# Kernel optimization log

Hardware: AMD Instinct MI355X
Metric: run time of the kernel (lower is better)

Reference implementation:

```python
import jax, jax.numpy as jnp
import numpy as np

N_NODES = 10000
N_EDGES = 160000
MUL = 64            # multiplicity of 0e and 1o in node features
AVG_NEIGH = 16.0    # avg_num_neighbors
N_BESSEL = 8
NUM_IRREPS = 4 * MUL  # 2*MUL scalars (0e) + 2*MUL vectors (1o) after concat+regroup

# e3nn normalize2mom constant for swish: 1/sqrt(E_{z~N(0,1)}[swish(z)^2])
_z, _w = np.polynomial.hermite_e.hermegauss(128)
_silu = _z / (1.0 + np.exp(-_z))
ACT_C = float(1.0 / np.sqrt(np.sum(_w * _silu ** 2) / np.sqrt(2.0 * np.pi)))


def bessel(x, n=N_BESSEL):
    # e3nn.bessel with x_max=1: sqrt(2) * sin(k*pi*x)/x, k=1..n
    k = jnp.arange(1, n + 1, dtype=x.dtype)
    xs = jnp.where(x == 0.0, 1.0, x)[:, None]
    return jnp.sqrt(2.0) * jnp.where(x[:, None] == 0.0, k * jnp.pi, jnp.sin(jnp.pi * k * xs) / xs)


def envelope(x):
    return jnp.where(x < 1.0, 1.0 - 28.0 * x ** 6 + 48.0 * x ** 7 - 21.0 * x ** 8, 0.0)


def mlp(x, Ws):
    # e3nn MultiLayerPerceptron: y = x @ W / sqrt(fan_in), normalized swish on hidden layers
    n = len(Ws)
    for i, W in enumerate(Ws):
        x = x @ W / jnp.sqrt(jnp.asarray(W.shape[0], x.dtype))
        if i < n - 1:
            x = ACT_C * jax.nn.swish(x)
    return x


def setup_inputs() -> dict:
    key = jax.random.key(0)
    ks = jax.random.split(key, 8)
    vectors = 0.35 * jax.random.normal(ks[0], (N_EDGES, 3), jnp.float32)
    node_scalars = jax.random.normal(ks[1], (N_NODES, MUL), jnp.float32)
    node_vectors = jax.random.normal(ks[2], (N_NODES, MUL, 3), jnp.float32)
    senders = jax.random.randint(ks[3], (N_EDGES,), 0, N_NODES)
    receivers = jax.random.randint(ks[4], (N_EDGES,), 0, N_NODES)
    W1 = jax.random.normal(ks[5], (N_BESSEL, 64), jnp.float32)
    W2 = jax.random.normal(ks[6], (64, 64), jnp.float32)
    W3 = jax.random.normal(ks[7], (64, NUM_IRREPS), jnp.float32)
    return dict(vectors=vectors, node_scalars=node_scalars, node_vectors=node_vectors,
                senders=senders, receivers=receivers, W1=W1, W2=W2, W3=W3)


def reference(vectors, node_scalars, node_vectors, senders, receivers, W1, W2, W3):
    lengths = jnp.linalg.norm(vectors, axis=-1, keepdims=True)        # [E,1]
    Y1 = jnp.sqrt(3.0) * vectors / lengths                            # component-normalized l=1 SH [E,3]

    # gather sender features
    m0 = node_scalars[senders]                                        # [E,MUL]   0e
    m1 = node_vectors[senders]                                        # [E,MUL,3] 1o

    # CG tensor product with Y1, filtered to target irreps (0e + 1o), component norm
    tp0 = jnp.einsum('eui,ei->eu', m1, Y1) / jnp.sqrt(3.0)            # 1o x 1o -> 0e
    tp1 = m0[:, :, None] * Y1[:, None, :]                             # 0e x 1o -> 1o

    s = jnp.concatenate([m0, tp0], axis=1)                            # [E,2*MUL]
    v = jnp.concatenate([m1, tp1], axis=1)                            # [E,2*MUL,3]

    # radial embedding -> per-irrep gates
    x = lengths[:, 0]
    radial = bessel(x) * envelope(x)[:, None]                         # [E,8]
    mix = mlp(radial, (W1, W2, W3))                                   # [E,4*MUL]

    s = s * mix[:, : 2 * MUL]
    v = v * mix[:, 2 * MUL :, None]

    # scatter-add to receivers
    out_s = jax.ops.segment_sum(s, receivers, num_segments=N_NODES)   # [N,2*MUL]
    out_v = jax.ops.segment_sum(v, receivers, num_segments=N_NODES)   # [N,2*MUL,3]
    inv = 1.0 / jnp.sqrt(AVG_NEIGH)
    return jnp.concatenate([out_s * inv, (out_v * inv).reshape(N_NODES, -1)], axis=1)
```

## Files before the change

kernel.cpp:

```cpp
#include <hip/hip_runtime.h>
#include <hip/hip_fp16.h>
#include <math.h>

#define N_NODES 10000
#define N_EDGES 160000
#define TBL_N 126
#define ACT_C 1.676518f
#define CAP 64
#define S3 1.7320508075688772f

#define SCAT_BLOCKS 625
#define CONV_BLOCKS 2500
#define TBL_BLOCKS  32
#define GATHER_BLOCKS 512
#define GATHER_THREADS 512

__device__ uint2  g_tbl[(TBL_N + 1) * 64];
__device__ uint2  g_nd2[N_NODES * 64];
__device__ int    g_cnt[N_NODES];
__device__ float4 g_bkt[N_NODES * CAP];

__device__ __forceinline__ float2 h2f(unsigned int v) {
    __half2 h = *(__half2*)&v;
    return __half22float2(h);
}

__global__ __launch_bounds__(256) void prep_scatter(
    const float* __restrict__ W1, const float* __restrict__ W2, const float* __restrict__ W3,
    const float* __restrict__ node_scalars, const float* __restrict__ node_vectors,
    const float* __restrict__ vectors, const int* __restrict__ senders,
    const int* __restrict__ receivers)
{
    const int bx = (int)blockIdx.x;
    const int tid = threadIdx.x;
    const int lane = tid & 63;
    const int wl = tid >> 6;

    if (bx < SCAT_BLOCKS) {
        int e = bx * 256 + tid;
        if (e < N_EDGES) {
            float vx = vectors[3 * e], vy = vectors[3 * e + 1], vz = vectors[3 * e + 2];
            float x2 = vx * vx + vy * vy + vz * vz;
            if (x2 < 1.0f) {
                float invx = rsqrtf(x2);
                float x = x2 * invx;
                float t = x * (float)TBL_N;
                int idx = (int)t;            if (idx > TBL_N - 1) idx = TBL_N - 1;
                int fr  = (int)((t - (float)idx) * 512.0f);  if (fr > 511) fr = 511;
                unsigned int bits = ((unsigned int)senders[e] << 16) |
                                    ((unsigned int)idx << 9) | (unsigned int)fr;
                int r = receivers[e];
                int slot = atomicAdd(&g_cnt[r], 1);
                if (slot < CAP)
                    g_bkt[(r << 6) + slot] =
                        make_float4(vx * invx, vy * invx, vz * invx, __uint_as_float(bits));
            }
        }
        return;
    }
    if (bx < SCAT_BLOCKS + CONV_BLOCKS) {
        int n = (bx - SCAT_BLOCKS) * 4 + wl;
        float m0 = node_scalars[n * 64 + lane];
        const float* p = node_vectors + n * 192 + 3 * lane;
        __half2 h01 = __floats2half2_rn(m0, p[0]);
        __half2 h23 = __floats2half2_rn(p[1], p[2]);
        uint2 r;
        r.x = *(unsigned int*)&h01;
        r.y = *(unsigned int*)&h23;
        g_nd2[n * 64 + lane] = r;
        return;
    }

    __shared__ float h[4][64];
    int wid = (bx - SCAT_BLOCKS - CONV_BLOCKS) * 4 + wl;
    if (wid > TBL_N) wid = TBL_N;
    const float x = (float)wid * (1.0f / (float)TBL_N);
    float x2 = x * x, x3 = x2 * x, x6 = x3 * x3;
    float env = (x < 1.0f) ? (1.0f - 28.0f * x6 + 48.0f * x6 * x - 21.0f * x6 * x2) : 0.0f;
    const float pi = 3.14159265358979f;
    float radial[8];
    #pragma unroll
    for (int k = 1; k <= 8; ++k) {
        float b = (x == 0.0f) ? ((float)k * pi) : (sinf(pi * (float)k * x) / x);
        radial[k - 1] = 1.41421356237f * b * env;
    }
    float acc = 0.0f;
    #pragma unroll
    for (int k = 0; k < 8; ++k) acc += radial[k] * W1[k * 64 + lane];
    acc *= 0.35355339059f;
    float a = ACT_C * acc / (1.0f + expf(-acc));
    h[wl][lane] = a;
    __syncthreads();
    acc = 0.0f;
    #pragma unroll 8
    for (int k = 0; k < 64; ++k) acc += h[wl][k] * W2[k * 64 + lane];
    acc *= 0.125f;
    a = ACT_C * acc / (1.0f + expf(-acc));
    __syncthreads();
    h[wl][lane] = a;
    __syncthreads();
    float m0 = 0.f, m1 = 0.f, m2 = 0.f, m3 = 0.f;
    #pragma unroll 4
    for (int k = 0; k < 64; ++k) {
        float hk = h[wl][k];
        const float* w = W3 + k * 256 + lane;
        m0 += hk * w[0];
        m1 += hk * w[64];
        m2 += hk * w[128];
        m3 += hk * w[192];
    }
    __half2 h01 = __floats2half2_rn(m0 * 0.125f, m1 * 0.125f);
    __half2 h23 = __floats2half2_rn(m2 * 0.125f, m3 * 0.125f);
    uint2 r;
    r.x = *(unsigned int*)&h01;
    r.y = *(unsigned int*)&h23;
    g_tbl[wid * 64 + lane] = r;
}

__device__ __forceinline__ void edge_math(uint2 q0, uint2 q1, uint2 nv, float f,
                                          float yx, float yy, float yz,
                                          float& accA, float& accB,
                                          float& aCx, float& aCy, float& aCz,
                                          float& aDx, float& aDy, float& aDz) {
    float2 a0 = h2f(q0.x);
    float2 b0 = h2f(q0.y);
    float2 a1 = h2f(q1.x);
    float2 b1 = h2f(q1.y);
    float2 p01 = h2f(nv.x);
    float2 p23 = h2f(nv.y);

    float mA = fmaf(f, a1.x - a0.x, a0.x);
    float mB = fmaf(f, a1.y - a0.y, a0.y);
    float mC = fmaf(f, b1.x - b0.x, b0.x);
    float mD = fmaf(f, b1.y - b0.y, b0.y);

    float m0u = p01.x, vx = p01.y, vy = p23.x, vzv = p23.y;
    float tp0 = fmaf(vx, yx, fmaf(vy, yy, vzv * yz));
    accA = fmaf(m0u, mA, accA);
    accB = fmaf(tp0, mB, accB);
    aCx = fmaf(mC, vx,  aCx);
    aCy = fmaf(mC, vy,  aCy);
    aCz = fmaf(mC, vzv, aCz);
    float cD = m0u * mD * S3;
    aDx = fmaf(cD, yx, aDx);
    aDy = fmaf(cD, yy, aDy);
    aDz = fmaf(cD, yz, aDz);
}

__global__ __launch_bounds__(GATHER_THREADS) void gather_kernel(float* __restrict__ out) {
    __shared__ uint2 tbl[(TBL_N + 1) * 64];
    const int tid = threadIdx.x;
    for (int i = tid; i < (TBL_N + 1) * 64; i += GATHER_THREADS)
        tbl[i] = g_tbl[i];
    __syncthreads();

    const int u = tid & 63;
    const int w = tid >> 6;
    const int nwaves = GATHER_BLOCKS * 8;

    for (int n = (int)blockIdx.x * 8 + w; n < N_NODES; n += nwaves) {
        int cnt = g_cnt[n]; if (cnt > CAP) cnt = CAP;
        const int base = n << 6;
        const float4 myrec = g_bkt[base + (u < cnt ? u : 0)];

        float accA = 0.f, accB = 0.f;
        float aCx = 0.f, aCy = 0.f, aCz = 0.f;
        float aDx = 0.f, aDy = 0.f, aDz = 0.f;

        int j = 0;
        for (; j + 4 <= cnt; j += 4) {
            uint2 q0[4], q1[4], nv[4];
            float yx[4], yy[4], yz[4], f[4];
            #pragma unroll
            for (int k = 0; k < 4; ++k) {
                int jj = j + k;
                yx[k] = __shfl(myrec.x, jj);
                yy[k] = __shfl(myrec.y, jj);
                yz[k] = __shfl(myrec.z, jj);
                unsigned int bits = __float_as_uint(__shfl(myrec.w, jj));
                int sv = (int)(bits >> 16);
                int i  = (int)((bits >> 9) & 127u);
                f[k] = (float)(bits & 511u) * (1.0f / 512.0f);
                q0[k] = tbl[i * 64 + u];
                q1[k] = tbl[i * 64 + 64 + u];
                nv[k] = g_nd2[sv * 64 + u];
            }
            #pragma unroll
            for (int k = 0; k < 4; ++k)
                edge_math(q0[k], q1[k], nv[k], f[k], yx[k], yy[k], yz[k],
                          accA, accB, aCx, aCy, aCz, aDx, aDy, aDz);
        }
        for (; j < cnt; ++j) {
            float yx = __shfl(myrec.x, j);
            float yy = __shfl(myrec.y, j);
            float yz = __shfl(myrec.z, j);
            unsigned int bits = __float_as_uint(__shfl(myrec.w, j));
            int sv = (int)(bits >> 16);
            int i  = (int)((bits >> 9) & 127u);
            float f = (float)(bits & 511u) * (1.0f / 512.0f);
            edge_math(tbl[i * 64 + u], tbl[i * 64 + 64 + u], g_nd2[sv * 64 + u], f,
                      yx, yy, yz, accA, accB, aCx, aCy, aCz, aDx, aDy, aDz);
        }

        const float inv = 0.25f;
        float* o = out + (size_t)n * 512;
        o[u]       = inv * accA;
        o[64 + u]  = inv * accB;
        o[128 + 3 * u + 0] = inv * aCx;
        o[128 + 3 * u + 1] = inv * aCy;
        o[128 + 3 * u + 2] = inv * aCz;
        o[320 + 3 * u + 0] = inv * aDx;
        o[320 + 3 * u + 1] = inv * aDy;
        o[320 + 3 * u + 2] = inv * aDz;
        if (u == 0) g_cnt[n] = 0;
    }
}

extern "C" void kernel_launch(void* const* d_in, const int* in_sizes, int n_in,
                              void* d_out, int out_size, void* d_ws, size_t ws_size,
                              hipStream_t stream) {
    const float* vectors      = (const float*)d_in[0];
    const float* node_scalars = (const float*)d_in[1];
    const float* node_vectors = (const float*)d_in[2];
    const int*   senders      = (const int*)d_in[3];
    const int*   receivers    = (const int*)d_in[4];
    const float* W1           = (const float*)d_in[5];
    const float* W2           = (const float*)d_in[6];
    const float* W3           = (const float*)d_in[7];
    float* out = (float*)d_out;

    prep_scatter<<<SCAT_BLOCKS + CONV_BLOCKS + TBL_BLOCKS, 256, 0, stream>>>(
        W1, W2, W3, node_scalars, node_vectors, vectors, senders, receivers);
    gather_kernel<<<GATHER_BLOCKS, GATHER_THREADS, 0, stream>>>(out);
}
```

Baseline: 45.29 us.

## Halve radial table resolution, double gather blocks, batch eight sender loads per step

The radial lookup table is cut from 127 to 64 rows, which halves the shared-memory footprint per gather block. Together with a launch-bounds occupancy hint and twice as many gather blocks, this is meant to fit more blocks per CU. The gather loop now issues eight sender-node loads up front, with clamped tail indices, before doing the edge math. The aim is more outstanding memory requests to hide gather latency. The coarser table interpolation reduces accuracy, and the bucket record is now loaded unconditionally even for slots beyond the count.

```diff
diff --git a/kernel.cpp b/kernel.cpp
--- a/kernel.cpp
+++ b/kernel.cpp
@@ -4,18 +4,19 @@
 
 #define N_NODES 10000
 #define N_EDGES 160000
-#define TBL_N 126
+#define TBL_N 63
+#define TBL_ROWS 64
 #define ACT_C 1.676518f
 #define CAP 64
 #define S3 1.7320508075688772f
 
 #define SCAT_BLOCKS 625
 #define CONV_BLOCKS 2500
-#define TBL_BLOCKS  32
-#define GATHER_BLOCKS 512
+#define TBL_BLOCKS  16
+#define GATHER_BLOCKS 1024
 #define GATHER_THREADS 512
 
-__device__ uint2  g_tbl[(TBL_N + 1) * 64];
+__device__ uint2  g_tbl[TBL_ROWS * 64];
 __device__ uint2  g_nd2[N_NODES * 64];
 __device__ int    g_cnt[N_NODES];
 __device__ float4 g_bkt[N_NODES * CAP];
@@ -73,7 +74,6 @@
 
     __shared__ float h[4][64];
     int wid = (bx - SCAT_BLOCKS - CONV_BLOCKS) * 4 + wl;
-    if (wid > TBL_N) wid = TBL_N;
     const float x = (float)wid * (1.0f / (float)TBL_N);
     float x2 = x * x, x3 = x2 * x, x6 = x3 * x3;
     float env = (x < 1.0f) ? (1.0f - 28.0f * x6 + 48.0f * x6 * x - 21.0f * x6 * x2) : 0.0f;
@@ -147,10 +147,10 @@
     aDz = fmaf(cD, yz, aDz);
 }
 
-__global__ __launch_bounds__(GATHER_THREADS) void gather_kernel(float* __restrict__ out) {
-    __shared__ uint2 tbl[(TBL_N + 1) * 64];
+__global__ __launch_bounds__(GATHER_THREADS, 8) void gather_kernel(float* __restrict__ out) {
+    __shared__ uint2 tbl[TBL_ROWS * 64];
     const int tid = threadIdx.x;
-    for (int i = tid; i < (TBL_N + 1) * 64; i += GATHER_THREADS)
+    for (int i = tid; i < TBL_ROWS * 64; i += GATHER_THREADS)
         tbl[i] = g_tbl[i];
     __syncthreads();
 
@@ -159,47 +159,37 @@
     const int nwaves = GATHER_BLOCKS * 8;
 
     for (int n = (int)blockIdx.x * 8 + w; n < N_NODES; n += nwaves) {
-        int cnt = g_cnt[n]; if (cnt > CAP) cnt = CAP;
         const int base = n << 6;
-        const float4 myrec = g_bkt[base + (u < cnt ? u : 0)];
+        int cnt = g_cnt[n];
+        const float4 myrec = g_bkt[base + u];
+        if (cnt > CAP) cnt = CAP;
 
         float accA = 0.f, accB = 0.f;
         float aCx = 0.f, aCy = 0.f, aCz = 0.f;
         float aDx = 0.f, aDy = 0.f, aDz = 0.f;
 
-        int j = 0;
-        for (; j + 4 <= cnt; j += 4) {
-            uint2 q0[4], q1[4], nv[4];
-            float yx[4], yy[4], yz[4], f[4];
+        for (int j = 0; j < cnt; j += 8) {
+            uint2 nv[8];
             #pragma unroll
-            for (int k = 0; k < 4; ++k) {
-                int jj = j + k;
-                yx[k] = __shfl(myrec.x, jj);
-                yy[k] = __shfl(myrec.y, jj);
-                yz[k] = __shfl(myrec.z, jj);
+            for (int k = 0; k < 8; ++k) {
+                int jj = j + k; if (jj >= cnt) jj = cnt - 1;
                 unsigned int bits = __float_as_uint(__shfl(myrec.w, jj));
-                int sv = (int)(bits >> 16);
-                int i  = (int)((bits >> 9) & 127u);
-                f[k] = (float)(bits & 511u) * (1.0f / 512.0f);
-                q0[k] = tbl[i * 64 + u];
-                q1[k] = tbl[i * 64 + 64 + u];
-                nv[k] = g_nd2[sv * 64 + u];
+                nv[k] = g_nd2[(int)(bits >> 16) * 64 + u];
             }
             #pragma unroll
-            for (int k = 0; k < 4; ++k)
-                edge_math(q0[k], q1[k], nv[k], f[k], yx[k], yy[k], yz[k],
-                          accA, accB, aCx, aCy, aCz, aDx, aDy, aDz);
-        }
-        for (; j < cnt; ++j) {
-            float yx = __shfl(myrec.x, j);
-            float yy = __shfl(myrec.y, j);
-            float yz = __shfl(myrec.z, j);
-            unsigned int bits = __float_as_uint(__shfl(myrec.w, j));
-            int sv = (int)(bits >> 16);
-            int i  = (int)((bits >> 9) & 127u);
-            float f = (float)(bits & 511u) * (1.0f / 512.0f);
-            edge_math(tbl[i * 64 + u], tbl[i * 64 + 64 + u], g_nd2[sv * 64 + u], f,
-                      yx, yy, yz, accA, accB, aCx, aCy, aCz, aDx, aDy, aDz);
+            for (int k = 0; k < 8; ++k) {
+                int jj = j + k;
+                if (jj < cnt) {
+                    float yx = __shfl(myrec.x, jj);
+                    float yy = __shfl(myrec.y, jj);
+                    float yz = __shfl(myrec.z, jj);
+                    unsigned int bits = __float_as_uint(__shfl(myrec.w, jj));
+                    int i = (int)((bits >> 9) & 127u);
+                    float f = (float)(bits & 511u) * (1.0f / 512.0f);
+                    edge_math(tbl[i * 64 + u], tbl[i * 64 + 64 + u], nv[k], f,
+                              yx, yy, yz, accA, accB, aCx, aCy, aCz, aDx, aDy, aDz);
+                }
+            }
         }
 
         const float inv = 0.25f;
```

Measured after the change: 45.48 us. About the same (+0.4%).

## Gather with one wave per node, drop LDS table staging, use scalar bucket loads

Applied to the files above, without the earlier changes.

The gather kernel now launches one wave per node (2500 blocks of 256 threads) instead of a persistent grid-stride loop. The per-block copy of the radial table into shared memory is removed, so table rows are read from global memory through the cache. Bucket records are read as wave-uniform loads (readfirstlane on node and count) rather than shuffled from per-lane registers. This removes the shared-memory fill and barrier at block start and the shuffle traffic, at the cost of table lookups going through L1/L2 instead of LDS.

```diff
diff --git a/kernel.cpp b/kernel.cpp
--- a/kernel.cpp
+++ b/kernel.cpp
@@ -5,6 +5,7 @@
 #define N_NODES 10000
 #define N_EDGES 160000
 #define TBL_N 126
+#define TBL_ROWS 127
 #define ACT_C 1.676518f
 #define CAP 64
 #define S3 1.7320508075688772f
@@ -12,10 +13,9 @@
 #define SCAT_BLOCKS 625
 #define CONV_BLOCKS 2500
 #define TBL_BLOCKS  32
-#define GATHER_BLOCKS 512
-#define GATHER_THREADS 512
-
-__device__ uint2  g_tbl[(TBL_N + 1) * 64];
+#define GATHER_BLOCKS 2500
+
+__device__ uint2  g_tbl[TBL_ROWS * 64];
 __device__ uint2  g_nd2[N_NODES * 64];
 __device__ int    g_cnt[N_NODES];
 __device__ float4 g_bkt[N_NODES * CAP];
@@ -147,73 +147,65 @@
     aDz = fmaf(cD, yz, aDz);
 }
 
-__global__ __launch_bounds__(GATHER_THREADS) void gather_kernel(float* __restrict__ out) {
-    __shared__ uint2 tbl[(TBL_N + 1) * 64];
-    const int tid = threadIdx.x;
-    for (int i = tid; i < (TBL_N + 1) * 64; i += GATHER_THREADS)
-        tbl[i] = g_tbl[i];
-    __syncthreads();
-
-    const int u = tid & 63;
-    const int w = tid >> 6;
-    const int nwaves = GATHER_BLOCKS * 8;
-
-    for (int n = (int)blockIdx.x * 8 + w; n < N_NODES; n += nwaves) {
-        int cnt = g_cnt[n]; if (cnt > CAP) cnt = CAP;
-        const int base = n << 6;
-        const float4 myrec = g_bkt[base + (u < cnt ? u : 0)];
-
-        float accA = 0.f, accB = 0.f;
-        float aCx = 0.f, aCy = 0.f, aCz = 0.f;
-        float aDx = 0.f, aDy = 0.f, aDz = 0.f;
-
-        int j = 0;
-        for (; j + 4 <= cnt; j += 4) {
-            uint2 q0[4], q1[4], nv[4];
-            float yx[4], yy[4], yz[4], f[4];
-            #pragma unroll
-            for (int k = 0; k < 4; ++k) {
-                int jj = j + k;
-                yx[k] = __shfl(myrec.x, jj);
-                yy[k] = __shfl(myrec.y, jj);
-                yz[k] = __shfl(myrec.z, jj);
-                unsigned int bits = __float_as_uint(__shfl(myrec.w, jj));
-                int sv = (int)(bits >> 16);
-                int i  = (int)((bits >> 9) & 127u);
-                f[k] = (float)(bits & 511u) * (1.0f / 512.0f);
-                q0[k] = tbl[i * 64 + u];
-                q1[k] = tbl[i * 64 + 64 + u];
-                nv[k] = g_nd2[sv * 64 + u];
-            }
-            #pragma unroll
-            for (int k = 0; k < 4; ++k)
-                edge_math(q0[k], q1[k], nv[k], f[k], yx[k], yy[k], yz[k],
-                          accA, accB, aCx, aCy, aCz, aDx, aDy, aDz);
+__global__ __launch_bounds__(256) void gather_kernel(float* __restrict__ out) {
+    const int u = threadIdx.x & 63;
+    const int nn = __builtin_amdgcn_readfirstlane((int)blockIdx.x * 4 + (threadIdx.x >> 6));
+
+    int cnt = __builtin_amdgcn_readfirstlane(g_cnt[nn]);
+    if (cnt > CAP) cnt = CAP;
+    const uint4* __restrict__ bkt = (const uint4*)(g_bkt + ((size_t)nn << 6));
+
+    float accA = 0.f, accB = 0.f;
+    float aCx = 0.f, aCy = 0.f, aCz = 0.f;
+    float aDx = 0.f, aDy = 0.f, aDz = 0.f;
+
+    int j = 0;
+    for (; j + 4 <= cnt; j += 4) {
+        uint2 q0[4], q1[4], nv[4];
+        float yx[4], yy[4], yz[4], f[4];
+        #pragma unroll
+        for (int k = 0; k < 4; ++k) {
+            uint4 r = bkt[j + k];
+            yx[k] = __uint_as_float(r.x);
+            yy[k] = __uint_as_float(r.y);
+            yz[k] = __uint_as_float(r.z);
+            unsigned int bits = r.w;
+            f[k] = (float)(bits & 511u) * (1.0f / 512.0f);
+            int i  = (int)((bits >> 9) & 127u);
+            int sv = (int)(bits >> 16);
+            nv[k] = g_nd2[sv * 64 + u];
+            q0[k] = g_tbl[i * 64 + u];
+            q1[k] = g_tbl[i * 64 + 64 + u];
         }
-        for (; j < cnt; ++j) {
-            float yx = __shfl(myrec.x, j);
-            float yy = __shfl(myrec.y, j);
-            float yz = __shfl(myrec.z, j);
-            unsigned int bits = __float_as_uint(__shfl(myrec.w, j));
-            int sv = (int)(bits >> 16);
-            int i  = (int)((bits >> 9) & 127u);
-            float f = (float)(bits & 511u) * (1.0f / 512.0f);
-            edge_math(tbl[i * 64 + u], tbl[i * 64 + 64 + u], g_nd2[sv * 64 + u], f,
-                      yx, yy, yz, accA, accB, aCx, aCy, aCz, aDx, aDy, aDz);
-        }
-
-        const float inv = 0.25f;
-        float* o = out + (size_t)n * 512;
-        o[u]       = inv * accA;
-        o[64 + u]  = inv * accB;
-        o[128 + 3 * u + 0] = inv * aCx;
-        o[128 + 3 * u + 1] = inv * aCy;
-        o[128 + 3 * u + 2] = inv * aCz;
-        o[320 + 3 * u + 0] = inv * aDx;
-        o[320 + 3 * u + 1] = inv * aDy;
-        o[320 + 3 * u + 2] = inv * aDz;
-        if (u == 0) g_cnt[n] = 0;
-    }
+        #pragma unroll
+        for (int k = 0; k < 4; ++k)
+            edge_math(q0[k], q1[k], nv[k], f[k], yx[k], yy[k], yz[k],
+                      accA, accB, aCx, aCy, aCz, aDx, aDy, aDz);
+    }
+    for (; j < cnt; ++j) {
+        uint4 r = bkt[j];
+        float yx = __uint_as_float(r.x);
+        float yy = __uint_as_float(r.y);
+        float yz = __uint_as_float(r.z);
+        unsigned int bits = r.w;
+        float f = (float)(bits & 511u) * (1.0f / 512.0f);
+        int i  = (int)((bits >> 9) & 127u);
+        int sv = (int)(bits >> 16);
+        edge_math(g_tbl[i * 64 + u], g_tbl[i * 64 + 64 + u], g_nd2[sv * 64 + u], f,
+                  yx, yy, yz, accA, accB, aCx, aCy, aCz, aDx, aDy, aDz);
+    }
+
+    const float inv = 0.25f;
+    float* o = out + (size_t)nn * 512;
+    o[u]       = inv * accA;
+    o[64 + u]  = inv * accB;
+    o[128 + 3 * u + 0] = inv * aCx;
+    o[128 + 3 * u + 1] = inv * aCy;
+    o[128 + 3 * u + 2] = inv * aCz;
+    o[320 + 3 * u + 0] = inv * aDx;
+    o[320 + 3 * u + 1] = inv * aDy;
+    o[320 + 3 * u + 2] = inv * aDz;
+    if (u == 0) g_cnt[nn] = 0;
 }
 
 extern "C" void kernel_launch(void* const* d_in, const int* in_sizes, int n_in,
@@ -231,5 +223,5 @@
 
     prep_scatter<<<SCAT_BLOCKS + CONV_BLOCKS + TBL_BLOCKS, 256, 0, stream>>>(
         W1, W2, W3, node_scalars, node_vectors, vectors, senders, receivers);
-    gather_kernel<<<GATHER_BLOCKS, GATHER_THREADS, 0, stream>>>(out);
-}
+    gather_kernel<<<GATHER_BLOCKS, 256, 0, stream>>>(out);
+}
```

Result: no change. 44.70 us (-1.3%).
